# Performance work log

Hardware: AMD Instinct MI355X
Metric: run time of the kernel (lower is better)

Reference implementation:

```python
import jax, jax.numpy as jnp
import numpy as np

CL = 32      # config.cl (latent width)
NOBJ = 32    # config.num_obj
N = 1024     # batch


def _linear_params(key, fan_in, fan_out):
    w = jax.random.normal(key, (fan_in, fan_out), dtype=jnp.float32) / np.sqrt(fan_in)
    b = jnp.full((fan_out,), 0.1, dtype=jnp.float32)
    return w, b


def setup_inputs() -> dict:
    key = jax.random.key(0)
    keys = jax.random.split(key, 16)
    inp = {"s": jax.random.normal(keys[0], (N, NOBJ, CL // 2), dtype=jnp.float32)}
    specs = [
        ("state_enc", [(CL // 2, CL)]),
        ("self", [(CL, CL), (CL, CL)]),
        ("rel", [(2 * CL + 1, 2 * CL), (2 * CL, CL), (CL, CL)]),
        ("att", [(2 * CL + 1, 2 * CL), (2 * CL, CL), (CL, 1)]),
        ("aff", [(CL, CL), (CL, CL), (CL, CL)]),
        ("out", [(2 * CL, CL), (CL, CL)]),
    ]
    k = 1
    for name, shapes in specs:
        for j, (fi, fo) in enumerate(shapes):
            w, b = _linear_params(keys[k], fi, fo)
            k += 1
            if len(shapes) == 1:
                inp[name + "_w"], inp[name + "_b"] = w, b
            else:
                inp[name + "_w" + str(j)], inp[name + "_b" + str(j)] = w, b
    inp["core_idx"] = 0
    return inp


def _forward(s, state_enc_w, state_enc_b,
             self_w0, self_b0, self_w1, self_b1,
             rel_w0, rel_b0, rel_w1, rel_b1, rel_w2, rel_b2,
             att_w0, att_b0, att_w1, att_b1, att_w2, att_b2,
             aff_w0, aff_b0, aff_w1, aff_b1, aff_w2, aff_b2,
             out_w0, out_b0, out_w1, out_b1):
    # state encoding; keep raw (x, y) positions in the first 2 channels
    enc = s @ state_enc_w + state_enc_b                      # (n, o, cl)
    s2 = jnp.concatenate([s[..., :2], enc[..., 2:]], axis=-1)  # (n, o, cl)

    # self dynamics (residual MLP)
    h1 = jax.nn.relu(s2 @ self_w0 + self_b0)
    self_dyn = h1 @ self_w1 + self_b1 + h1                   # (n, o, cl)

    # pairwise squared distance over first two channels
    pos = s2[..., :2]
    diff = pos[:, :, None, :] - pos[:, None, :, :]           # (n, o, o, 2)
    dist = jnp.sum(diff * diff, axis=-1)                     # (n, o, o)

    # first layer of the edge MLPs applied to cat(obj_i, obj_j, dist) without
    # materializing the (n, o, o, 2cl+1) concat: split weight into W_i|W_j|w_d
    def pair_first(W, b):
        a = s2 @ W[:CL]                                      # (n, o, H)
        c = s2 @ W[CL:2 * CL]                                # (n, o, H)
        return a[:, :, None, :] + c[:, None, :, :] + dist[..., None] * W[2 * CL] + b

    # relation core (residual on last layer)
    rel1 = jax.nn.relu(pair_first(rel_w0, rel_b0))           # (n, o, o, 2cl)
    rel2 = jax.nn.relu(rel1 @ rel_w1 + rel_b1)               # (n, o, o, cl)
    rel_f = rel2 @ rel_w2 + rel_b2 + rel2                    # (n, o, o, cl)

    # attention net -> exp (unnormalized attention)
    att = jax.nn.relu(pair_first(att_w0, att_b0))
    att = jax.nn.relu(att @ att_w1 + att_b1)
    att = jnp.exp(att @ att_w2 + att_b2)                     # (n, o, o, 1)

    diag_mask = (1.0 - jnp.eye(NOBJ, dtype=s2.dtype))[None, :, :, None]
    rel_dyn = jnp.sum(rel_f * diag_mask * att, axis=2)       # (n, o, cl)

    dyn = self_dyn + rel_dyn

    # affector (tanh residual MLP)
    aff1 = jnp.tanh(dyn @ aff_w0 + aff_b0)
    aff2 = jnp.tanh(aff1 @ aff_w1 + aff_b1) + aff1
    aff3 = aff2 @ aff_w2 + aff_b2

    # output head
    aff_s = jnp.concatenate([aff3, s2], axis=-1)             # (n, o, 2cl)
    o1 = jnp.tanh(aff_s @ out_w0 + out_b0)
    result = o1 @ out_w1 + out_b1 + o1                       # (n, o, cl)
    return result


def reference(s, state_enc_w, state_enc_b,
              self_w0, self_b0, self_w1, self_b1,
              rel_w0, rel_b0, rel_w1, rel_b1, rel_w2, rel_b2,
              att_w0, att_b0, att_w1, att_b1, att_w2, att_b2,
              aff_w0, aff_b0, aff_w1, aff_b1, aff_w2, aff_b2,
              out_w0, out_b0, out_w1, out_b1, core_idx):
    # core_idx selects one of 3 identical cores in the original; only core 0
    # is materialized here (forward uses a single core).
    del core_idx
    return _forward(s, state_enc_w, state_enc_b,
                    self_w0, self_b0, self_w1, self_b1,
                    rel_w0, rel_b0, rel_w1, rel_b1, rel_w2, rel_b2,
                    att_w0, att_b0, att_w1, att_b1, att_w2, att_b2,
                    aff_w0, aff_b0, aff_w1, aff_b1, aff_w2, aff_b2,
                    out_w0, out_b0, out_w1, out_b1)
```

## Files before the change

kernel.cpp:

```cpp
#include <hip/hip_runtime.h>
#include <stdint.h>


enum : int {
  ENC_W  = 0,     ENC_B  = 512,
  SELF_W0 = 544,  SELF_B0 = 1568, SELF_W1 = 1600, SELF_B1 = 2624,
  REL_W0 = 2656,  REL_B0 = 6816,  REL_W1 = 6880,  REL_B1 = 8928,
  REL_W2 = 8960,  REL_B2 = 9984,
  ATT_W0 = 10016, ATT_B0 = 14176, ATT_W1 = 14240, ATT_B1 = 16288,
  ATT_W2 = 16320, ATT_B2 = 16352,
  AFF_W0 = 16356, AFF_B0 = 17380, AFF_W1 = 17412, AFF_B1 = 18436,
  AFF_W2 = 18468, AFF_B2 = 19492,
  OUT_W0 = 19524, OUT_B0 = 21572, OUT_W1 = 21604, OUT_B1 = 22628,
  W_FLAG = 22660,
  W_TOTAL = 22661
};

__device__ __forceinline__ float bf2f(uint16_t h) {
  union { uint32_t u; float f; } v; v.u = ((uint32_t)h) << 16; return v.f;
}
__device__ __forceinline__ uint16_t f2bf(float f) {
  union { float f; uint32_t u; } v; v.f = f;
  uint32_t r = (v.u + 0x7fffu + ((v.u >> 16) & 1u)) >> 16;
  return (uint16_t)r;
}

struct ConvArgs {
  const void* src[28];
  const uint32_t* probe;
  int size[28];
  int off[28];
};

__global__ void dyn_conv_kernel(ConvArgs a, float* __restrict__ W) {
  const int t = blockIdx.x;
  const bool is_fp32 = (*a.probe == 0x3DCCCCCDu);
  const int cnt = a.size[t];
  float* d = W + a.off[t];
  if (is_fp32) {
    const float* s = (const float*)a.src[t];
    for (int e = threadIdx.x; e < cnt; e += blockDim.x) d[e] = s[e];
  } else {
    const uint16_t* s = (const uint16_t*)a.src[t];
    for (int e = threadIdx.x; e < cnt; e += blockDim.x) d[e] = bf2f(s[e]);
  }
  if (t == 0 && threadIdx.x == 0) W[W_FLAG] = is_fp32 ? 1.f : 0.f;
}

struct ArenaPair {
  float pa[32][68];
  float pc[32][68];
};
struct ArenaPost {
  float rd[32][36];
  float t1[32][36];
  float t2[32][36];
};
struct ArenaEarly {
  float s[32][16];
  float h1[32][33];
};
union ArenaU {
  ArenaPair a;
  ArenaPost b;
  ArenaEarly c;
};

__global__ __launch_bounds__(256, 2) void dyn_main_kernel(
    const void* __restrict__ Sv,
    const float* __restrict__ Wf,
    void* __restrict__ OUTv)
{
  __shared__ __align__(16) ArenaU u;
  __shared__ float sh_s2[32][33];
  __shared__ float sh_dist[32][33];
  __shared__ float sh_sd[32][33];
  __shared__ float sh_wdr[64];
  __shared__ float sh_wda[64];
  __shared__ __align__(16) float sh_wtA[2048];
  __shared__ __align__(16) float sh_wtB[2048];
  __shared__ float sh_misc[100];

  const int tid = threadIdx.x;
  const int n   = blockIdx.x;
  const int i8  = tid >> 3;
  const int l8  = tid & 7;
  const int m0  = l8 << 2;
  const int jg  = l8 & 3;
  const int h16 = (l8 >> 2) << 4;
  const int h4  = (l8 >> 2) << 2;

  const bool is_fp32 = (Wf[W_FLAG] != 0.f);

  const float4* wtA4 = (const float4*)sh_wtA;
  const float4* wtB4 = (const float4*)sh_wtB;

  auto stage = [&](float* dst, int off, int n4) {
    const float4* src = (const float4*)(Wf + off);
    float4* d4 = (float4*)dst;
    for (int q = tid; q < n4; q += 256) d4[q] = src[q];
  };

  {
    const int e = tid * 2;
    if (is_fp32) {
      const float* sp = (const float*)Sv + (size_t)n * 512;
      u.c.s[e >> 4][e & 15]             = sp[e];
      u.c.s[(e + 1) >> 4][(e + 1) & 15] = sp[e + 1];
    } else {
      const uint16_t* sp = (const uint16_t*)Sv + (size_t)n * 512;
      u.c.s[e >> 4][e & 15]             = bf2f(sp[e]);
      u.c.s[(e + 1) >> 4][(e + 1) & 15] = bf2f(sp[e + 1]);
    }
    stage(sh_wtA, ENC_W, 128);
  }
  __syncthreads();

  {
    float e0 = Wf[ENC_B + m0 + 0], e1 = Wf[ENC_B + m0 + 1];
    float e2 = Wf[ENC_B + m0 + 2], e3 = Wf[ENC_B + m0 + 3];
    #pragma unroll
    for (int c = 0; c < 16; ++c) {
      const float sc = u.c.s[i8][c];
      const float4 w = wtA4[c * 8 + l8];
      e0 = fmaf(sc, w.x, e0); e1 = fmaf(sc, w.y, e1);
      e2 = fmaf(sc, w.z, e2); e3 = fmaf(sc, w.w, e3);
    }
    if (m0 == 0) { e0 = u.c.s[i8][0]; e1 = u.c.s[i8][1]; }
    sh_s2[i8][m0 + 0] = e0; sh_s2[i8][m0 + 1] = e1;
    sh_s2[i8][m0 + 2] = e2; sh_s2[i8][m0 + 3] = e3;
    stage(sh_wtB, SELF_W0, 256);
  }
  __syncthreads();

  {
    const float xi = sh_s2[i8][0], yi = sh_s2[i8][1];
    #pragma unroll
    for (int q = 0; q < 4; ++q) {
      const int j = m0 + q;
      const float dx = xi - sh_s2[j][0];
      const float dy = yi - sh_s2[j][1];
      sh_dist[i8][j] = dx * dx + dy * dy;
    }
  }
  {
    float a0 = Wf[SELF_B0 + m0 + 0], a1 = Wf[SELF_B0 + m0 + 1];
    float a2 = Wf[SELF_B0 + m0 + 2], a3 = Wf[SELF_B0 + m0 + 3];
    #pragma unroll
    for (int k = 0; k < 32; ++k) {
      const float x = sh_s2[i8][k];
      const float4 w = wtB4[k * 8 + l8];
      a0 = fmaf(x, w.x, a0); a1 = fmaf(x, w.y, a1);
      a2 = fmaf(x, w.z, a2); a3 = fmaf(x, w.w, a3);
    }
    u.c.h1[i8][m0 + 0] = fmaxf(a0, 0.f); u.c.h1[i8][m0 + 1] = fmaxf(a1, 0.f);
    u.c.h1[i8][m0 + 2] = fmaxf(a2, 0.f); u.c.h1[i8][m0 + 3] = fmaxf(a3, 0.f);
    stage(sh_wtA, SELF_W1, 256);
  }
  __syncthreads();

  {
    float a0 = Wf[SELF_B1 + m0 + 0], a1 = Wf[SELF_B1 + m0 + 1];
    float a2 = Wf[SELF_B1 + m0 + 2], a3 = Wf[SELF_B1 + m0 + 3];
    #pragma unroll
    for (int k = 0; k < 32; ++k) {
      const float x = u.c.h1[i8][k];
      const float4 w = wtA4[k * 8 + l8];
      a0 = fmaf(x, w.x, a0); a1 = fmaf(x, w.y, a1);
      a2 = fmaf(x, w.z, a2); a3 = fmaf(x, w.w, a3);
    }
    sh_sd[i8][m0 + 0] = a0 + u.c.h1[i8][m0 + 0];
    sh_sd[i8][m0 + 1] = a1 + u.c.h1[i8][m0 + 1];
    sh_sd[i8][m0 + 2] = a2 + u.c.h1[i8][m0 + 2];
    sh_sd[i8][m0 + 3] = a3 + u.c.h1[i8][m0 + 3];
  }
  __syncthreads();

  auto precompute_ac = [&](int W0base, int B0base) {
    const int arr = tid >> 7;
    const int row = (tid >> 2) & 31;
    const int k0  = (tid & 3) * 16;
    const float* bb = Wf + B0base + k0;
    const float bs = (arr == 0) ? 1.f : 0.f;
    float acc[16];
    #pragma unroll
    for (int kk = 0; kk < 16; ++kk) acc[kk] = bs * bb[kk];
    const float* wb = Wf + W0base + arr * 2048 + k0;
    for (int c = 0; c < 32; ++c) {
      const float sc = sh_s2[row][c];
      const float* w = wb + c * 64;
      #pragma unroll
      for (int kk = 0; kk < 16; kk += 4) {
        const float4 wv = *(const float4*)&w[kk];
        acc[kk + 0] = fmaf(sc, wv.x, acc[kk + 0]);
        acc[kk + 1] = fmaf(sc, wv.y, acc[kk + 1]);
        acc[kk + 2] = fmaf(sc, wv.z, acc[kk + 2]);
        acc[kk + 3] = fmaf(sc, wv.w, acc[kk + 3]);
      }
    }
    float* dst = (arr == 0) ? &u.a.pa[row][k0] : &u.a.pc[row][k0];
    #pragma unroll
    for (int kk = 0; kk < 16; kk += 4)
      *(float4*)&dst[kk] = make_float4(acc[kk], acc[kk+1], acc[kk+2], acc[kk+3]);
  };

  if (tid < 64)        sh_wdr[tid]      = Wf[REL_W0 + 64 * 64 + tid];
  else if (tid < 128)  sh_wda[tid - 64] = Wf[ATT_W0 + 64 * 64 + (tid - 64)];
  stage(sh_wtB, ATT_W1, 512);
  if (tid < 97)
    sh_misc[tid] = Wf[tid < 32 ? REL_B1 + tid
                    : tid < 64 ? ATT_B1 + (tid - 32)
                    : tid < 96 ? ATT_W2 + (tid - 64) : ATT_B2];
  precompute_ac(ATT_W0, ATT_B0);
  __syncthreads();

  stage(sh_wtA, REL_W1, 512);
  auto att_pair2 = [&](int p) -> float2 {
    asm volatile("" ::: "memory");
    const int j1 = jg + 8 * p;
    const int j2 = jg + 4 + 8 * p;
    const float d1 = sh_dist[i8][j1];
    const float d2 = sh_dist[i8][j2];
    const float4* A  = (const float4*)&u.a.pa[i8][0];
    const float4* C1 = (const float4*)&u.a.pc[j1][0];
    const float4* C2 = (const float4*)&u.a.pc[j2][0];
    const float4* D  = (const float4*)&sh_wda[0];
    float v1[16], v2[16];
    #pragma unroll
    for (int m = 0; m < 16; ++m) { v1[m] = sh_misc[32 + h16 + m]; v2[m] = v1[m]; }
    #pragma unroll 1
    for (int kq = 0; kq < 16; ++kq) {
      const float4 av = A[kq], c1 = C1[kq], c2 = C2[kq], wv = D[kq];
      const float x0 = fmaxf(fmaf(d1, wv.x, av.x + c1.x), 0.f);
      const float x1 = fmaxf(fmaf(d1, wv.y, av.y + c1.y), 0.f);
      const float x2 = fmaxf(fmaf(d1, wv.z, av.z + c1.z), 0.f);
      const float x3 = fmaxf(fmaf(d1, wv.w, av.w + c1.w), 0.f);
      const float y0 = fmaxf(fmaf(d2, wv.x, av.x + c2.x), 0.f);
      const float y1 = fmaxf(fmaf(d2, wv.y, av.y + c2.y), 0.f);
      const float y2 = fmaxf(fmaf(d2, wv.z, av.z + c2.z), 0.f);
      const float y3 = fmaxf(fmaf(d2, wv.w, av.w + c2.w), 0.f);
      const float4* wb = wtB4 + kq * 32 + h4;
      #pragma unroll
      for (int mq = 0; mq < 4; ++mq) {
        const float4 w0 = wb[mq], w1 = wb[8+mq], w2 = wb[16+mq], w3 = wb[24+mq];
        float t;
        t = fmaf(x0, w0.x, v1[mq*4+0]); t = fmaf(x1, w1.x, t);
        t = fmaf(x2, w2.x, t);          v1[mq*4+0] = fmaf(x3, w3.x, t);
        t = fmaf(y0, w0.x, v2[mq*4+0]); t = fmaf(y1, w1.x, t);
        t = fmaf(y2, w2.x, t);          v2[mq*4+0] = fmaf(y3, w3.x, t);
        t = fmaf(x0, w0.y, v1[mq*4+1]); t = fmaf(x1, w1.y, t);
        t = fmaf(x2, w2.y, t);          v1[mq*4+1] = fmaf(x3, w3.y, t);
        t = fmaf(y0, w0.y, v2[mq*4+1]); t = fmaf(y1, w1.y, t);
        t = fmaf(y2, w2.y, t);          v2[mq*4+1] = fmaf(y3, w3.y, t);
        t = fmaf(x0, w0.z, v1[mq*4+2]); t = fmaf(x1, w1.z, t);
        t = fmaf(x2, w2.z, t);          v1[mq*4+2] = fmaf(x3, w3.z, t);
        t = fmaf(y0, w0.z, v2[mq*4+2]); t = fmaf(y1, w1.z, t);
        t = fmaf(y2, w2.z, t);          v2[mq*4+2] = fmaf(y3, w3.z, t);
        t = fmaf(x0, w0.w, v1[mq*4+3]); t = fmaf(x1, w1.w, t);
        t = fmaf(x2, w2.w, t);          v1[mq*4+3] = fmaf(x3, w3.w, t);
        t = fmaf(y0, w0.w, v2[mq*4+3]); t = fmaf(y1, w1.w, t);
        t = fmaf(y2, w2.w, t);          v2[mq*4+3] = fmaf(y3, w3.w, t);
      }
    }
    float la0 = 0.f, la1 = 0.f, lb0 = 0.f, lb1 = 0.f;
    #pragma unroll
    for (int k = 0; k < 16; k += 2) {
      la0 = fmaf(fmaxf(v1[k + 0], 0.f), sh_misc[64 + h16 + k + 0], la0);
      la1 = fmaf(fmaxf(v1[k + 1], 0.f), sh_misc[64 + h16 + k + 1], la1);
      lb0 = fmaf(fmaxf(v2[k + 0], 0.f), sh_misc[64 + h16 + k + 0], lb0);
      lb1 = fmaf(fmaxf(v2[k + 1], 0.f), sh_misc[64 + h16 + k + 1], lb1);
    }
    float lg1 = la0 + la1;
    float lg2 = lb0 + lb1;
    lg1 += __shfl_xor(lg1, 4);
    lg2 += __shfl_xor(lg2, 4);
    lg1 += sh_misc[96];
    lg2 += sh_misc[96];
    float2 r;
    r.x = (j1 == i8) ? 0.f : expf(lg1);
    r.y = (j2 == i8) ? 0.f : expf(lg2);
    return r;
  };
  const float2 ep0 = att_pair2(0);
  const float2 ep1 = att_pair2(1);
  const float2 ep2 = att_pair2(2);
  const float2 ep3 = att_pair2(3);
  float E = ((ep0.x + ep0.y) + (ep1.x + ep1.y))
          + ((ep2.x + ep2.y) + (ep3.x + ep3.y));
  __syncthreads();

  precompute_ac(REL_W0, REL_B0);
  stage(sh_wtB, REL_W2, 256);
  __syncthreads();

  float g[16];
  #pragma unroll
  for (int m = 0; m < 16; ++m) g[m] = 0.f;

  auto rel_pair2 = [&](int p, float e1, float e2) {
    asm volatile("" ::: "memory");
    const int j1 = jg + 8 * p;
    const int j2 = jg + 4 + 8 * p;
    const float d1 = sh_dist[i8][j1];
    const float d2 = sh_dist[i8][j2];
    const float4* A  = (const float4*)&u.a.pa[i8][0];
    const float4* C1 = (const float4*)&u.a.pc[j1][0];
    const float4* C2 = (const float4*)&u.a.pc[j2][0];
    const float4* D  = (const float4*)&sh_wdr[0];
    float v1[16], v2[16];
    #pragma unroll
    for (int m = 0; m < 16; ++m) { v1[m] = sh_misc[h16 + m]; v2[m] = v1[m]; }
    #pragma unroll 1
    for (int kq = 0; kq < 16; ++kq) {
      const float4 av = A[kq], c1 = C1[kq], c2 = C2[kq], wv = D[kq];
      const float x0 = fmaxf(fmaf(d1, wv.x, av.x + c1.x), 0.f);
      const float x1 = fmaxf(fmaf(d1, wv.y, av.y + c1.y), 0.f);
      const float x2 = fmaxf(fmaf(d1, wv.z, av.z + c1.z), 0.f);
      const float x3 = fmaxf(fmaf(d1, wv.w, av.w + c1.w), 0.f);
      const float y0 = fmaxf(fmaf(d2, wv.x, av.x + c2.x), 0.f);
      const float y1 = fmaxf(fmaf(d2, wv.y, av.y + c2.y), 0.f);
      const float y2 = fmaxf(fmaf(d2, wv.z, av.z + c2.z), 0.f);
      const float y3 = fmaxf(fmaf(d2, wv.w, av.w + c2.w), 0.f);
      const float4* wb = wtA4 + kq * 32 + h4;
      #pragma unroll
      for (int mq = 0; mq < 4; ++mq) {
        const float4 w0 = wb[mq], w1 = wb[8+mq], w2 = wb[16+mq], w3 = wb[24+mq];
        float t;
        t = fmaf(x0, w0.x, v1[mq*4+0]); t = fmaf(x1, w1.x, t);
        t = fmaf(x2, w2.x, t);          v1[mq*4+0] = fmaf(x3, w3.x, t);
        t = fmaf(y0, w0.x, v2[mq*4+0]); t = fmaf(y1, w1.x, t);
        t = fmaf(y2, w2.x, t);          v2[mq*4+0] = fmaf(y3, w3.x, t);
        t = fmaf(x0, w0.y, v1[mq*4+1]); t = fmaf(x1, w1.y, t);
        t = fmaf(x2, w2.y, t);          v1[mq*4+1] = fmaf(x3, w3.y, t);
        t = fmaf(y0, w0.y, v2[mq*4+1]); t = fmaf(y1, w1.y, t);
        t = fmaf(y2, w2.y, t);          v2[mq*4+1] = fmaf(y3, w3.y, t);
        t = fmaf(x0, w0.z, v1[mq*4+2]); t = fmaf(x1, w1.z, t);
        t = fmaf(x2, w2.z, t);          v1[mq*4+2] = fmaf(x3, w3.z, t);
        t = fmaf(y0, w0.z, v2[mq*4+2]); t = fmaf(y1, w1.z, t);
        t = fmaf(y2, w2.z, t);          v2[mq*4+2] = fmaf(y3, w3.z, t);
        t = fmaf(x0, w0.w, v1[mq*4+3]); t = fmaf(x1, w1.w, t);
        t = fmaf(x2, w2.w, t);          v1[mq*4+3] = fmaf(x3, w3.w, t);
        t = fmaf(y0, w0.w, v2[mq*4+3]); t = fmaf(y1, w1.w, t);
        t = fmaf(y2, w2.w, t);          v2[mq*4+3] = fmaf(y3, w3.w, t);
      }
    }
    #pragma unroll
    for (int m = 0; m < 16; ++m) {
      g[m] = fmaf(e1, fmaxf(v1[m], 0.f), g[m]);
      g[m] = fmaf(e2, fmaxf(v2[m], 0.f), g[m]);
    }
  };
  rel_pair2(0, ep0.x, ep0.y);
  rel_pair2(1, ep1.x, ep1.y);
  rel_pair2(2, ep2.x, ep2.y);
  rel_pair2(3, ep3.x, ep3.y);

  #pragma unroll
  for (int m = 0; m < 16; ++m) {
    float vv = g[m];
    vv += __shfl_xor(vv, 1);
    vv += __shfl_xor(vv, 2);
    g[m] = vv;
  }
  E += __shfl_xor(E, 1);
  E += __shfl_xor(E, 2);
  __syncthreads();
  if (l8 == 0) {
    #pragma unroll
    for (int q = 0; q < 4; ++q)
      *(float4*)&u.b.t1[i8][q * 4] =
          make_float4(g[q * 4], g[q * 4 + 1], g[q * 4 + 2], g[q * 4 + 3]);
    u.b.t1[i8][32] = E;
  } else if (l8 == 4) {
    #pragma unroll
    for (int q = 0; q < 4; ++q)
      *(float4*)&u.b.t1[i8][16 + q * 4] =
          make_float4(g[q * 4], g[q * 4 + 1], g[q * 4 + 2], g[q * 4 + 3]);
  }
  __syncthreads();

  {
    stage(sh_wtA, AFF_W0, 256);
    const float Ei = u.b.t1[i8][32];
    float a0 = fmaf(Ei, Wf[REL_B2 + m0 + 0], u.b.t1[i8][m0 + 0]);
    float a1 = fmaf(Ei, Wf[REL_B2 + m0 + 1], u.b.t1[i8][m0 + 1]);
    float a2 = fmaf(Ei, Wf[REL_B2 + m0 + 2], u.b.t1[i8][m0 + 2]);
    float a3 = fmaf(Ei, Wf[REL_B2 + m0 + 3], u.b.t1[i8][m0 + 3]);
    #pragma unroll
    for (int k = 0; k < 32; ++k) {
      const float x = u.b.t1[i8][k];
      const float4 w = wtB4[k * 8 + l8];
      a0 = fmaf(x, w.x, a0); a1 = fmaf(x, w.y, a1);
      a2 = fmaf(x, w.z, a2); a3 = fmaf(x, w.w, a3);
    }
    __syncthreads();
    u.b.rd[i8][m0 + 0] = a0; u.b.rd[i8][m0 + 1] = a1;
    u.b.rd[i8][m0 + 2] = a2; u.b.rd[i8][m0 + 3] = a3;
  }
  __syncthreads();

  {
    stage(sh_wtB, AFF_W1, 256);
    float a0 = Wf[AFF_B0 + m0 + 0], a1 = Wf[AFF_B0 + m0 + 1];
    float a2 = Wf[AFF_B0 + m0 + 2], a3 = Wf[AFF_B0 + m0 + 3];
    #pragma unroll
    for (int k = 0; k < 32; ++k) {
      const float x = sh_sd[i8][k] + u.b.rd[i8][k];
      const float4 w = wtA4[k * 8 + l8];
      a0 = fmaf(x, w.x, a0); a1 = fmaf(x, w.y, a1);
      a2 = fmaf(x, w.z, a2); a3 = fmaf(x, w.w, a3);
    }
    u.b.t1[i8][m0 + 0] = tanhf(a0); u.b.t1[i8][m0 + 1] = tanhf(a1);
    u.b.t1[i8][m0 + 2] = tanhf(a2); u.b.t1[i8][m0 + 3] = tanhf(a3);
  }
  __syncthreads();

  {
    stage(sh_wtA, AFF_W2, 256);
    float a0 = Wf[AFF_B1 + m0 + 0], a1 = Wf[AFF_B1 + m0 + 1];
    float a2 = Wf[AFF_B1 + m0 + 2], a3 = Wf[AFF_B1 + m0 + 3];
    #pragma unroll
    for (int k = 0; k < 32; ++k) {
      const float x = u.b.t1[i8][k];
      const float4 w = wtB4[k * 8 + l8];
      a0 = fmaf(x, w.x, a0); a1 = fmaf(x, w.y, a1);
      a2 = fmaf(x, w.z, a2); a3 = fmaf(x, w.w, a3);
    }
    u.b.t2[i8][m0 + 0] = tanhf(a0) + u.b.t1[i8][m0 + 0];
    u.b.t2[i8][m0 + 1] = tanhf(a1) + u.b.t1[i8][m0 + 1];
    u.b.t2[i8][m0 + 2] = tanhf(a2) + u.b.t1[i8][m0 + 2];
    u.b.t2[i8][m0 + 3] = tanhf(a3) + u.b.t1[i8][m0 + 3];
  }
  __syncthreads();

  {
    stage(sh_wtB, OUT_W0, 512);
    float a0 = Wf[AFF_B2 + m0 + 0], a1 = Wf[AFF_B2 + m0 + 1];
    float a2 = Wf[AFF_B2 + m0 + 2], a3 = Wf[AFF_B2 + m0 + 3];
    #pragma unroll
    for (int k = 0; k < 32; ++k) {
      const float x = u.b.t2[i8][k];
      const float4 w = wtA4[k * 8 + l8];
      a0 = fmaf(x, w.x, a0); a1 = fmaf(x, w.y, a1);
      a2 = fmaf(x, w.z, a2); a3 = fmaf(x, w.w, a3);
    }
    u.b.t1[i8][m0 + 0] = a0; u.b.t1[i8][m0 + 1] = a1;
    u.b.t1[i8][m0 + 2] = a2; u.b.t1[i8][m0 + 3] = a3;
  }
  __syncthreads();

  {
    stage(sh_wtA, OUT_W1, 256);
    float a0 = Wf[OUT_B0 + m0 + 0], a1 = Wf[OUT_B0 + m0 + 1];
    float a2 = Wf[OUT_B0 + m0 + 2], a3 = Wf[OUT_B0 + m0 + 3];
    #pragma unroll
    for (int k = 0; k < 32; ++k) {
      const float x1 = u.b.t1[i8][k];
      const float4 wa = wtB4[k * 8 + l8];
      a0 = fmaf(x1, wa.x, a0); a1 = fmaf(x1, wa.y, a1);
      a2 = fmaf(x1, wa.z, a2); a3 = fmaf(x1, wa.w, a3);
      const float x2 = sh_s2[i8][k];
      const float4 wbv = wtB4[256 + k * 8 + l8];
      a0 = fmaf(x2, wbv.x, a0); a1 = fmaf(x2, wbv.y, a1);
      a2 = fmaf(x2, wbv.z, a2); a3 = fmaf(x2, wbv.w, a3);
    }
    u.b.t2[i8][m0 + 0] = tanhf(a0); u.b.t2[i8][m0 + 1] = tanhf(a1);
    u.b.t2[i8][m0 + 2] = tanhf(a2); u.b.t2[i8][m0 + 3] = tanhf(a3);
  }
  __syncthreads();

  {
    float a0 = Wf[OUT_B1 + m0 + 0], a1 = Wf[OUT_B1 + m0 + 1];
    float a2 = Wf[OUT_B1 + m0 + 2], a3 = Wf[OUT_B1 + m0 + 3];
    #pragma unroll
    for (int k = 0; k < 32; ++k) {
      const float x = u.b.t2[i8][k];
      const float4 w = wtA4[k * 8 + l8];
      a0 = fmaf(x, w.x, a0); a1 = fmaf(x, w.y, a1);
      a2 = fmaf(x, w.z, a2); a3 = fmaf(x, w.w, a3);
    }
    a0 += u.b.t2[i8][m0 + 0]; a1 += u.b.t2[i8][m0 + 1];
    a2 += u.b.t2[i8][m0 + 2]; a3 += u.b.t2[i8][m0 + 3];
    const size_t idx = (size_t)n * 1024 + i8 * 32 + m0;
    if (is_fp32) {
      *(float4*)&((float*)OUTv)[idx] = make_float4(a0, a1, a2, a3);
    } else {
      ushort4 r;
      r.x = f2bf(a0); r.y = f2bf(a1); r.z = f2bf(a2); r.w = f2bf(a3);
      *(ushort4*)&((uint16_t*)OUTv)[idx] = r;
    }
  }
}

extern "C" void kernel_launch(void* const* d_in, const int* in_sizes, int n_in,
                              void* d_out, int out_size, void* d_ws, size_t ws_size,
                              hipStream_t stream) {
  (void)in_sizes; (void)n_in; (void)out_size; (void)ws_size;
  static const int sizes[28] = {
    512, 32, 1024, 32, 1024, 32,
    4160, 64, 2048, 32, 1024, 32,
    4160, 64, 2048, 32, 32, 1,
    1024, 32, 1024, 32, 1024, 32,
    2048, 32, 1024, 32};
  static const int offs[28] = {
    ENC_W, ENC_B, SELF_W0, SELF_B0, SELF_W1, SELF_B1,
    REL_W0, REL_B0, REL_W1, REL_B1, REL_W2, REL_B2,
    ATT_W0, ATT_B0, ATT_W1, ATT_B1, ATT_W2, ATT_B2,
    AFF_W0, AFF_B0, AFF_W1, AFF_B1, AFF_W2, AFF_B2,
    OUT_W0, OUT_B0, OUT_W1, OUT_B1};

  ConvArgs ca;
  for (int i = 0; i < 28; ++i) {
    ca.src[i]  = d_in[1 + i];
    ca.size[i] = sizes[i];
    ca.off[i]  = offs[i];
  }
  ca.probe = (const uint32_t*)d_in[2];
  float* W = (float*)d_ws;
  hipLaunchKernelGGL(dyn_conv_kernel, dim3(28), dim3(256), 0, stream, ca, W);
  hipLaunchKernelGGL(dyn_main_kernel, dim3(1024), dim3(256), 0, stream,
                     d_in[0], (const float*)W, d_out);
}
```

Before: 324.1 us.

## Split fused kernel into pairwise and tail kernels via workspace

Splits the single fused per-batch kernel into two. The first computes the encoding, self dynamics and the attention-weighted pairwise aggregation, writing s2, self_dyn, g and E to global workspace. The second reads these back and runs the rel/aff/out MLP tail. The aim is to shrink shared memory and register footprint per kernel so occupancy improves, at the cost of an extra launch and about 12 MB of global traffic. The original fused kernel is kept as a fallback when the workspace is too small.

```diff
diff --git a/kernel.cpp b/kernel.cpp
--- a/kernel.cpp
+++ b/kernel.cpp
@@ -15,6 +15,14 @@
   W_FLAG = 22660,
   W_TOTAL = 22661
 };
+enum : int {
+  WS_S2 = 22664,
+  WS_SD = WS_S2 + 1048576,
+  WS_G  = WS_SD + 1048576,
+  WS_E  = WS_G  + 1048576,
+  WS_TOTAL_F = WS_E + 32768
+};
+static const size_t WS_NEED_BYTES = (size_t)WS_TOTAL_F * 4;
 
 __device__ __forceinline__ float bf2f(uint16_t h) {
   union { uint32_t u; float f; } v; v.u = ((uint32_t)h) << 16; return v.f;
@@ -66,15 +74,13 @@
   ArenaEarly c;
 };
 
-__global__ __launch_bounds__(256, 2) void dyn_main_kernel(
-    const void* __restrict__ Sv,
-    const float* __restrict__ Wf,
-    void* __restrict__ OUTv)
+__global__ __launch_bounds__(256, 2) void dyn_pair_kernel(
+    const void* __restrict__ Sv, const float* __restrict__ Wf,
+    float* __restrict__ WS)
 {
   __shared__ __align__(16) ArenaU u;
   __shared__ float sh_s2[32][33];
   __shared__ float sh_dist[32][33];
-  __shared__ float sh_sd[32][33];
   __shared__ float sh_wdr[64];
   __shared__ float sh_wda[64];
   __shared__ __align__(16) float sh_wtA[2048];
@@ -91,7 +97,6 @@
   const int h4  = (l8 >> 2) << 2;
 
   const bool is_fp32 = (Wf[W_FLAG] != 0.f);
-
   const float4* wtA4 = (const float4*)sh_wtA;
   const float4* wtB4 = (const float4*)sh_wtB;
 
@@ -129,6 +134,8 @@
     if (m0 == 0) { e0 = u.c.s[i8][0]; e1 = u.c.s[i8][1]; }
     sh_s2[i8][m0 + 0] = e0; sh_s2[i8][m0 + 1] = e1;
     sh_s2[i8][m0 + 2] = e2; sh_s2[i8][m0 + 3] = e3;
+    *(float4*)&WS[WS_S2 + (size_t)n * 1024 + i8 * 32 + m0] =
+        make_float4(e0, e1, e2, e3);
     stage(sh_wtB, SELF_W0, 256);
   }
   __syncthreads();
@@ -169,10 +176,9 @@
       a0 = fmaf(x, w.x, a0); a1 = fmaf(x, w.y, a1);
       a2 = fmaf(x, w.z, a2); a3 = fmaf(x, w.w, a3);
     }
-    sh_sd[i8][m0 + 0] = a0 + u.c.h1[i8][m0 + 0];
-    sh_sd[i8][m0 + 1] = a1 + u.c.h1[i8][m0 + 1];
-    sh_sd[i8][m0 + 2] = a2 + u.c.h1[i8][m0 + 2];
-    sh_sd[i8][m0 + 3] = a3 + u.c.h1[i8][m0 + 3];
+    *(float4*)&WS[WS_SD + (size_t)n * 1024 + i8 * 32 + m0] =
+        make_float4(a0 + u.c.h1[i8][m0 + 0], a1 + u.c.h1[i8][m0 + 1],
+                    a2 + u.c.h1[i8][m0 + 2], a3 + u.c.h1[i8][m0 + 3]);
   }
   __syncthreads();
 
@@ -290,7 +296,6 @@
   __syncthreads();
 
   precompute_ac(REL_W0, REL_B0);
-  stage(sh_wtB, REL_W2, 256);
   __syncthreads();
 
   float g[16];
@@ -364,6 +369,469 @@
   }
   E += __shfl_xor(E, 1);
   E += __shfl_xor(E, 2);
+  if (l8 == 0) {
+    #pragma unroll
+    for (int q = 0; q < 4; ++q)
+      *(float4*)&WS[WS_G + (size_t)n * 1024 + i8 * 32 + q * 4] =
+          make_float4(g[q * 4], g[q * 4 + 1], g[q * 4 + 2], g[q * 4 + 3]);
+    WS[WS_E + n * 32 + i8] = E;
+  } else if (l8 == 4) {
+    #pragma unroll
+    for (int q = 0; q < 4; ++q)
+      *(float4*)&WS[WS_G + (size_t)n * 1024 + i8 * 32 + 16 + q * 4] =
+          make_float4(g[q * 4], g[q * 4 + 1], g[q * 4 + 2], g[q * 4 + 3]);
+  }
+}
+
+__global__ __launch_bounds__(256, 2) void dyn_tail_kernel(
+    const float* __restrict__ Wf, const float* __restrict__ WS,
+    void* __restrict__ OUTv)
+{
+  __shared__ __align__(16) ArenaPost b;
+  __shared__ float sh_s2[32][33];
+  __shared__ float sh_sd[32][33];
+  __shared__ __align__(16) float sh_wtA[2048];
+  __shared__ __align__(16) float sh_wtB[2048];
+
+  const int tid = threadIdx.x;
+  const int n   = blockIdx.x;
+  const int i8  = tid >> 3;
+  const int l8  = tid & 7;
+  const int m0  = l8 << 2;
+
+  const bool is_fp32 = (Wf[W_FLAG] != 0.f);
+  const float4* wtA4 = (const float4*)sh_wtA;
+  const float4* wtB4 = (const float4*)sh_wtB;
+
+  auto stage = [&](float* dst, int off, int n4) {
+    const float4* src = (const float4*)(Wf + off);
+    float4* d4 = (float4*)dst;
+    for (int q = tid; q < n4; q += 256) d4[q] = src[q];
+  };
+
+  {
+    const int idx = tid << 2;
+    const int ii = idx >> 5, kk = idx & 31;
+    const float4 vs = *(const float4*)&WS[WS_S2 + (size_t)n * 1024 + idx];
+    sh_s2[ii][kk + 0] = vs.x; sh_s2[ii][kk + 1] = vs.y;
+    sh_s2[ii][kk + 2] = vs.z; sh_s2[ii][kk + 3] = vs.w;
+    const float4 vd = *(const float4*)&WS[WS_SD + (size_t)n * 1024 + idx];
+    sh_sd[ii][kk + 0] = vd.x; sh_sd[ii][kk + 1] = vd.y;
+    sh_sd[ii][kk + 2] = vd.z; sh_sd[ii][kk + 3] = vd.w;
+    const float4 vg = *(const float4*)&WS[WS_G + (size_t)n * 1024 + idx];
+    b.t1[ii][kk + 0] = vg.x; b.t1[ii][kk + 1] = vg.y;
+    b.t1[ii][kk + 2] = vg.z; b.t1[ii][kk + 3] = vg.w;
+    if (tid < 32) b.t1[tid][32] = WS[WS_E + n * 32 + tid];
+    stage(sh_wtB, REL_W2, 256);
+  }
+  __syncthreads();
+
+  {
+    stage(sh_wtA, AFF_W0, 256);
+    const float Ei = b.t1[i8][32];
+    float a0 = fmaf(Ei, Wf[REL_B2 + m0 + 0], b.t1[i8][m0 + 0]);
+    float a1 = fmaf(Ei, Wf[REL_B2 + m0 + 1], b.t1[i8][m0 + 1]);
+    float a2 = fmaf(Ei, Wf[REL_B2 + m0 + 2], b.t1[i8][m0 + 2]);
+    float a3 = fmaf(Ei, Wf[REL_B2 + m0 + 3], b.t1[i8][m0 + 3]);
+    #pragma unroll
+    for (int k = 0; k < 32; ++k) {
+      const float x = b.t1[i8][k];
+      const float4 w = wtB4[k * 8 + l8];
+      a0 = fmaf(x, w.x, a0); a1 = fmaf(x, w.y, a1);
+      a2 = fmaf(x, w.z, a2); a3 = fmaf(x, w.w, a3);
+    }
+    __syncthreads();
+    b.rd[i8][m0 + 0] = a0; b.rd[i8][m0 + 1] = a1;
+    b.rd[i8][m0 + 2] = a2; b.rd[i8][m0 + 3] = a3;
+  }
+  __syncthreads();
+
+  {
+    stage(sh_wtB, AFF_W1, 256);
+    float a0 = Wf[AFF_B0 + m0 + 0], a1 = Wf[AFF_B0 + m0 + 1];
+    float a2 = Wf[AFF_B0 + m0 + 2], a3 = Wf[AFF_B0 + m0 + 3];
+    #pragma unroll
+    for (int k = 0; k < 32; ++k) {
+      const float x = sh_sd[i8][k] + b.rd[i8][k];
+      const float4 w = wtA4[k * 8 + l8];
+      a0 = fmaf(x, w.x, a0); a1 = fmaf(x, w.y, a1);
+      a2 = fmaf(x, w.z, a2); a3 = fmaf(x, w.w, a3);
+    }
+    b.t1[i8][m0 + 0] = tanhf(a0); b.t1[i8][m0 + 1] = tanhf(a1);
+    b.t1[i8][m0 + 2] = tanhf(a2); b.t1[i8][m0 + 3] = tanhf(a3);
+  }
+  __syncthreads();
+
+  {
+    stage(sh_wtA, AFF_W2, 256);
+    float a0 = Wf[AFF_B1 + m0 + 0], a1 = Wf[AFF_B1 + m0 + 1];
+    float a2 = Wf[AFF_B1 + m0 + 2], a3 = Wf[AFF_B1 + m0 + 3];
+    #pragma unroll
+    for (int k = 0; k < 32; ++k) {
+      const float x = b.t1[i8][k];
+      const float4 w = wtB4[k * 8 + l8];
+      a0 = fmaf(x, w.x, a0); a1 = fmaf(x, w.y, a1);
+      a2 = fmaf(x, w.z, a2); a3 = fmaf(x, w.w, a3);
+    }
+    b.t2[i8][m0 + 0] = tanhf(a0) + b.t1[i8][m0 + 0];
+    b.t2[i8][m0 + 1] = tanhf(a1) + b.t1[i8][m0 + 1];
+    b.t2[i8][m0 + 2] = tanhf(a2) + b.t1[i8][m0 + 2];
+    b.t2[i8][m0 + 3] = tanhf(a3) + b.t1[i8][m0 + 3];
+  }
+  __syncthreads();
+
+  {
+    stage(sh_wtB, OUT_W0, 512);
+    float a0 = Wf[AFF_B2 + m0 + 0], a1 = Wf[AFF_B2 + m0 + 1];
+    float a2 = Wf[AFF_B2 + m0 + 2], a3 = Wf[AFF_B2 + m0 + 3];
+    #pragma unroll
+    for (int k = 0; k < 32; ++k) {
+      const float x = b.t2[i8][k];
+      const float4 w = wtA4[k * 8 + l8];
+      a0 = fmaf(x, w.x, a0); a1 = fmaf(x, w.y, a1);
+      a2 = fmaf(x, w.z, a2); a3 = fmaf(x, w.w, a3);
+    }
+    b.t1[i8][m0 + 0] = a0; b.t1[i8][m0 + 1] = a1;
+    b.t1[i8][m0 + 2] = a2; b.t1[i8][m0 + 3] = a3;
+  }
+  __syncthreads();
+
+  {
+    stage(sh_wtA, OUT_W1, 256);
+    float a0 = Wf[OUT_B0 + m0 + 0], a1 = Wf[OUT_B0 + m0 + 1];
+    float a2 = Wf[OUT_B0 + m0 + 2], a3 = Wf[OUT_B0 + m0 + 3];
+    #pragma unroll
+    for (int k = 0; k < 32; ++k) {
+      const float x1 = b.t1[i8][k];
+      const float4 wa = wtB4[k * 8 + l8];
+      a0 = fmaf(x1, wa.x, a0); a1 = fmaf(x1, wa.y, a1);
+      a2 = fmaf(x1, wa.z, a2); a3 = fmaf(x1, wa.w, a3);
+      const float x2 = sh_s2[i8][k];
+      const float4 wbv = wtB4[256 + k * 8 + l8];
+      a0 = fmaf(x2, wbv.x, a0); a1 = fmaf(x2, wbv.y, a1);
+      a2 = fmaf(x2, wbv.z, a2); a3 = fmaf(x2, wbv.w, a3);
+    }
+    b.t2[i8][m0 + 0] = tanhf(a0); b.t2[i8][m0 + 1] = tanhf(a1);
+    b.t2[i8][m0 + 2] = tanhf(a2); b.t2[i8][m0 + 3] = tanhf(a3);
+  }
+  __syncthreads();
+
+  {
+    float a0 = Wf[OUT_B1 + m0 + 0], a1 = Wf[OUT_B1 + m0 + 1];
+    float a2 = Wf[OUT_B1 + m0 + 2], a3 = Wf[OUT_B1 + m0 + 3];
+    #pragma unroll
+    for (int k = 0; k < 32; ++k) {
+      const float x = b.t2[i8][k];
+      const float4 w = wtA4[k * 8 + l8];
+      a0 = fmaf(x, w.x, a0); a1 = fmaf(x, w.y, a1);
+      a2 = fmaf(x, w.z, a2); a3 = fmaf(x, w.w, a3);
+    }
+    a0 += b.t2[i8][m0 + 0]; a1 += b.t2[i8][m0 + 1];
+    a2 += b.t2[i8][m0 + 2]; a3 += b.t2[i8][m0 + 3];
+    const size_t idx = (size_t)n * 1024 + i8 * 32 + m0;
+    if (is_fp32) {
+      *(float4*)&((float*)OUTv)[idx] = make_float4(a0, a1, a2, a3);
+    } else {
+      ushort4 r;
+      r.x = f2bf(a0); r.y = f2bf(a1); r.z = f2bf(a2); r.w = f2bf(a3);
+      *(ushort4*)&((uint16_t*)OUTv)[idx] = r;
+    }
+  }
+}
+
+__global__ __launch_bounds__(256, 2) void dyn_main_kernel(
+    const void* __restrict__ Sv, const float* __restrict__ Wf,
+    void* __restrict__ OUTv)
+{
+  __shared__ __align__(16) ArenaU u;
+  __shared__ float sh_s2[32][33];
+  __shared__ float sh_dist[32][33];
+  __shared__ float sh_sd[32][33];
+  __shared__ float sh_wdr[64];
+  __shared__ float sh_wda[64];
+  __shared__ __align__(16) float sh_wtA[2048];
+  __shared__ __align__(16) float sh_wtB[2048];
+  __shared__ float sh_misc[100];
+
+  const int tid = threadIdx.x;
+  const int n   = blockIdx.x;
+  const int i8  = tid >> 3;
+  const int l8  = tid & 7;
+  const int m0  = l8 << 2;
+  const int jg  = l8 & 3;
+  const int h16 = (l8 >> 2) << 4;
+  const int h4  = (l8 >> 2) << 2;
+
+  const bool is_fp32 = (Wf[W_FLAG] != 0.f);
+  const float4* wtA4 = (const float4*)sh_wtA;
+  const float4* wtB4 = (const float4*)sh_wtB;
+
+  auto stage = [&](float* dst, int off, int n4) {
+    const float4* src = (const float4*)(Wf + off);
+    float4* d4 = (float4*)dst;
+    for (int q = tid; q < n4; q += 256) d4[q] = src[q];
+  };
+
+  {
+    const int e = tid * 2;
+    if (is_fp32) {
+      const float* sp = (const float*)Sv + (size_t)n * 512;
+      u.c.s[e >> 4][e & 15]             = sp[e];
+      u.c.s[(e + 1) >> 4][(e + 1) & 15] = sp[e + 1];
+    } else {
+      const uint16_t* sp = (const uint16_t*)Sv + (size_t)n * 512;
+      u.c.s[e >> 4][e & 15]             = bf2f(sp[e]);
+      u.c.s[(e + 1) >> 4][(e + 1) & 15] = bf2f(sp[e + 1]);
+    }
+    stage(sh_wtA, ENC_W, 128);
+  }
+  __syncthreads();
+  {
+    float e0 = Wf[ENC_B + m0 + 0], e1 = Wf[ENC_B + m0 + 1];
+    float e2 = Wf[ENC_B + m0 + 2], e3 = Wf[ENC_B + m0 + 3];
+    #pragma unroll
+    for (int c = 0; c < 16; ++c) {
+      const float sc = u.c.s[i8][c];
+      const float4 w = wtA4[c * 8 + l8];
+      e0 = fmaf(sc, w.x, e0); e1 = fmaf(sc, w.y, e1);
+      e2 = fmaf(sc, w.z, e2); e3 = fmaf(sc, w.w, e3);
+    }
+    if (m0 == 0) { e0 = u.c.s[i8][0]; e1 = u.c.s[i8][1]; }
+    sh_s2[i8][m0 + 0] = e0; sh_s2[i8][m0 + 1] = e1;
+    sh_s2[i8][m0 + 2] = e2; sh_s2[i8][m0 + 3] = e3;
+    stage(sh_wtB, SELF_W0, 256);
+  }
+  __syncthreads();
+  {
+    const float xi = sh_s2[i8][0], yi = sh_s2[i8][1];
+    #pragma unroll
+    for (int q = 0; q < 4; ++q) {
+      const int j = m0 + q;
+      const float dx = xi - sh_s2[j][0];
+      const float dy = yi - sh_s2[j][1];
+      sh_dist[i8][j] = dx * dx + dy * dy;
+    }
+  }
+  {
+    float a0 = Wf[SELF_B0 + m0 + 0], a1 = Wf[SELF_B0 + m0 + 1];
+    float a2 = Wf[SELF_B0 + m0 + 2], a3 = Wf[SELF_B0 + m0 + 3];
+    #pragma unroll
+    for (int k = 0; k < 32; ++k) {
+      const float x = sh_s2[i8][k];
+      const float4 w = wtB4[k * 8 + l8];
+      a0 = fmaf(x, w.x, a0); a1 = fmaf(x, w.y, a1);
+      a2 = fmaf(x, w.z, a2); a3 = fmaf(x, w.w, a3);
+    }
+    u.c.h1[i8][m0 + 0] = fmaxf(a0, 0.f); u.c.h1[i8][m0 + 1] = fmaxf(a1, 0.f);
+    u.c.h1[i8][m0 + 2] = fmaxf(a2, 0.f); u.c.h1[i8][m0 + 3] = fmaxf(a3, 0.f);
+    stage(sh_wtA, SELF_W1, 256);
+  }
+  __syncthreads();
+  {
+    float a0 = Wf[SELF_B1 + m0 + 0], a1 = Wf[SELF_B1 + m0 + 1];
+    float a2 = Wf[SELF_B1 + m0 + 2], a3 = Wf[SELF_B1 + m0 + 3];
+    #pragma unroll
+    for (int k = 0; k < 32; ++k) {
+      const float x = u.c.h1[i8][k];
+      const float4 w = wtA4[k * 8 + l8];
+      a0 = fmaf(x, w.x, a0); a1 = fmaf(x, w.y, a1);
+      a2 = fmaf(x, w.z, a2); a3 = fmaf(x, w.w, a3);
+    }
+    sh_sd[i8][m0 + 0] = a0 + u.c.h1[i8][m0 + 0];
+    sh_sd[i8][m0 + 1] = a1 + u.c.h1[i8][m0 + 1];
+    sh_sd[i8][m0 + 2] = a2 + u.c.h1[i8][m0 + 2];
+    sh_sd[i8][m0 + 3] = a3 + u.c.h1[i8][m0 + 3];
+  }
+  __syncthreads();
+
+  auto precompute_ac = [&](int W0base, int B0base) {
+    const int arr = tid >> 7;
+    const int row = (tid >> 2) & 31;
+    const int k0  = (tid & 3) * 16;
+    const float* bb = Wf + B0base + k0;
+    const float bs = (arr == 0) ? 1.f : 0.f;
+    float acc[16];
+    #pragma unroll
+    for (int kk = 0; kk < 16; ++kk) acc[kk] = bs * bb[kk];
+    const float* wb = Wf + W0base + arr * 2048 + k0;
+    for (int c = 0; c < 32; ++c) {
+      const float sc = sh_s2[row][c];
+      const float* w = wb + c * 64;
+      #pragma unroll
+      for (int kk = 0; kk < 16; kk += 4) {
+        const float4 wv = *(const float4*)&w[kk];
+        acc[kk + 0] = fmaf(sc, wv.x, acc[kk + 0]);
+        acc[kk + 1] = fmaf(sc, wv.y, acc[kk + 1]);
+        acc[kk + 2] = fmaf(sc, wv.z, acc[kk + 2]);
+        acc[kk + 3] = fmaf(sc, wv.w, acc[kk + 3]);
+      }
+    }
+    float* dst = (arr == 0) ? &u.a.pa[row][k0] : &u.a.pc[row][k0];
+    #pragma unroll
+    for (int kk = 0; kk < 16; kk += 4)
+      *(float4*)&dst[kk] = make_float4(acc[kk], acc[kk+1], acc[kk+2], acc[kk+3]);
+  };
+
+  if (tid < 64)        sh_wdr[tid]      = Wf[REL_W0 + 64 * 64 + tid];
+  else if (tid < 128)  sh_wda[tid - 64] = Wf[ATT_W0 + 64 * 64 + (tid - 64)];
+  stage(sh_wtB, ATT_W1, 512);
+  if (tid < 97)
+    sh_misc[tid] = Wf[tid < 32 ? REL_B1 + tid
+                    : tid < 64 ? ATT_B1 + (tid - 32)
+                    : tid < 96 ? ATT_W2 + (tid - 64) : ATT_B2];
+  precompute_ac(ATT_W0, ATT_B0);
+  __syncthreads();
+
+  stage(sh_wtA, REL_W1, 512);
+  auto att_pair2 = [&](int p) -> float2 {
+    asm volatile("" ::: "memory");
+    const int j1 = jg + 8 * p;
+    const int j2 = jg + 4 + 8 * p;
+    const float d1 = sh_dist[i8][j1];
+    const float d2 = sh_dist[i8][j2];
+    const float4* A  = (const float4*)&u.a.pa[i8][0];
+    const float4* C1 = (const float4*)&u.a.pc[j1][0];
+    const float4* C2 = (const float4*)&u.a.pc[j2][0];
+    const float4* D  = (const float4*)&sh_wda[0];
+    float v1[16], v2[16];
+    #pragma unroll
+    for (int m = 0; m < 16; ++m) { v1[m] = sh_misc[32 + h16 + m]; v2[m] = v1[m]; }
+    #pragma unroll 1
+    for (int kq = 0; kq < 16; ++kq) {
+      const float4 av = A[kq], c1 = C1[kq], c2 = C2[kq], wv = D[kq];
+      const float x0 = fmaxf(fmaf(d1, wv.x, av.x + c1.x), 0.f);
+      const float x1 = fmaxf(fmaf(d1, wv.y, av.y + c1.y), 0.f);
+      const float x2 = fmaxf(fmaf(d1, wv.z, av.z + c1.z), 0.f);
+      const float x3 = fmaxf(fmaf(d1, wv.w, av.w + c1.w), 0.f);
+      const float y0 = fmaxf(fmaf(d2, wv.x, av.x + c2.x), 0.f);
+      const float y1 = fmaxf(fmaf(d2, wv.y, av.y + c2.y), 0.f);
+      const float y2 = fmaxf(fmaf(d2, wv.z, av.z + c2.z), 0.f);
+      const float y3 = fmaxf(fmaf(d2, wv.w, av.w + c2.w), 0.f);
+      const float4* wb = wtB4 + kq * 32 + h4;
+      #pragma unroll
+      for (int mq = 0; mq < 4; ++mq) {
+        const float4 w0 = wb[mq], w1 = wb[8+mq], w2 = wb[16+mq], w3 = wb[24+mq];
+        float t;
+        t = fmaf(x0, w0.x, v1[mq*4+0]); t = fmaf(x1, w1.x, t);
+        t = fmaf(x2, w2.x, t);          v1[mq*4+0] = fmaf(x3, w3.x, t);
+        t = fmaf(y0, w0.x, v2[mq*4+0]); t = fmaf(y1, w1.x, t);
+        t = fmaf(y2, w2.x, t);          v2[mq*4+0] = fmaf(y3, w3.x, t);
+        t = fmaf(x0, w0.y, v1[mq*4+1]); t = fmaf(x1, w1.y, t);
+        t = fmaf(x2, w2.y, t);          v1[mq*4+1] = fmaf(x3, w3.y, t);
+        t = fmaf(y0, w0.y, v2[mq*4+1]); t = fmaf(y1, w1.y, t);
+        t = fmaf(y2, w2.y, t);          v2[mq*4+1] = fmaf(y3, w3.y, t);
+        t = fmaf(x0, w0.z, v1[mq*4+2]); t = fmaf(x1, w1.z, t);
+        t = fmaf(x2, w2.z, t);          v1[mq*4+2] = fmaf(x3, w3.z, t);
+        t = fmaf(y0, w0.z, v2[mq*4+2]); t = fmaf(y1, w1.z, t);
+        t = fmaf(y2, w2.z, t);          v2[mq*4+2] = fmaf(y3, w3.z, t);
+        t = fmaf(x0, w0.w, v1[mq*4+3]); t = fmaf(x1, w1.w, t);
+        t = fmaf(x2, w2.w, t);          v1[mq*4+3] = fmaf(x3, w3.w, t);
+        t = fmaf(y0, w0.w, v2[mq*4+3]); t = fmaf(y1, w1.w, t);
+        t = fmaf(y2, w2.w, t);          v2[mq*4+3] = fmaf(y3, w3.w, t);
+      }
+    }
+    float la0 = 0.f, la1 = 0.f, lb0 = 0.f, lb1 = 0.f;
+    #pragma unroll
+    for (int k = 0; k < 16; k += 2) {
+      la0 = fmaf(fmaxf(v1[k + 0], 0.f), sh_misc[64 + h16 + k + 0], la0);
+      la1 = fmaf(fmaxf(v1[k + 1], 0.f), sh_misc[64 + h16 + k + 1], la1);
+      lb0 = fmaf(fmaxf(v2[k + 0], 0.f), sh_misc[64 + h16 + k + 0], lb0);
+      lb1 = fmaf(fmaxf(v2[k + 1], 0.f), sh_misc[64 + h16 + k + 1], lb1);
+    }
+    float lg1 = la0 + la1;
+    float lg2 = lb0 + lb1;
+    lg1 += __shfl_xor(lg1, 4);
+    lg2 += __shfl_xor(lg2, 4);
+    lg1 += sh_misc[96];
+    lg2 += sh_misc[96];
+    float2 r;
+    r.x = (j1 == i8) ? 0.f : expf(lg1);
+    r.y = (j2 == i8) ? 0.f : expf(lg2);
+    return r;
+  };
+  const float2 ep0 = att_pair2(0);
+  const float2 ep1 = att_pair2(1);
+  const float2 ep2 = att_pair2(2);
+  const float2 ep3 = att_pair2(3);
+  float E = ((ep0.x + ep0.y) + (ep1.x + ep1.y))
+          + ((ep2.x + ep2.y) + (ep3.x + ep3.y));
+  __syncthreads();
+
+  precompute_ac(REL_W0, REL_B0);
+  stage(sh_wtB, REL_W2, 256);
+  __syncthreads();
+
+  float g[16];
+  #pragma unroll
+  for (int m = 0; m < 16; ++m) g[m] = 0.f;
+
+  auto rel_pair2 = [&](int p, float e1, float e2) {
+    asm volatile("" ::: "memory");
+    const int j1 = jg + 8 * p;
+    const int j2 = jg + 4 + 8 * p;
+    const float d1 = sh_dist[i8][j1];
+    const float d2 = sh_dist[i8][j2];
+    const float4* A  = (const float4*)&u.a.pa[i8][0];
+    const float4* C1 = (const float4*)&u.a.pc[j1][0];
+    const float4* C2 = (const float4*)&u.a.pc[j2][0];
+    const float4* D  = (const float4*)&sh_wdr[0];
+    float v1[16], v2[16];
+    #pragma unroll
+    for (int m = 0; m < 16; ++m) { v1[m] = sh_misc[h16 + m]; v2[m] = v1[m]; }
+    #pragma unroll 1
+    for (int kq = 0; kq < 16; ++kq) {
+      const float4 av = A[kq], c1 = C1[kq], c2 = C2[kq], wv = D[kq];
+      const float x0 = fmaxf(fmaf(d1, wv.x, av.x + c1.x), 0.f);
+      const float x1 = fmaxf(fmaf(d1, wv.y, av.y + c1.y), 0.f);
+      const float x2 = fmaxf(fmaf(d1, wv.z, av.z + c1.z), 0.f);
+      const float x3 = fmaxf(fmaf(d1, wv.w, av.w + c1.w), 0.f);
+      const float y0 = fmaxf(fmaf(d2, wv.x, av.x + c2.x), 0.f);
+      const float y1 = fmaxf(fmaf(d2, wv.y, av.y + c2.y), 0.f);
+      const float y2 = fmaxf(fmaf(d2, wv.z, av.z + c2.z), 0.f);
+      const float y3 = fmaxf(fmaf(d2, wv.w, av.w + c2.w), 0.f);
+      const float4* wb = wtA4 + kq * 32 + h4;
+      #pragma unroll
+      for (int mq = 0; mq < 4; ++mq) {
+        const float4 w0 = wb[mq], w1 = wb[8+mq], w2 = wb[16+mq], w3 = wb[24+mq];
+        float t;
+        t = fmaf(x0, w0.x, v1[mq*4+0]); t = fmaf(x1, w1.x, t);
+        t = fmaf(x2, w2.x, t);          v1[mq*4+0] = fmaf(x3, w3.x, t);
+        t = fmaf(y0, w0.x, v2[mq*4+0]); t = fmaf(y1, w1.x, t);
+        t = fmaf(y2, w2.x, t);          v2[mq*4+0] = fmaf(y3, w3.x, t);
+        t = fmaf(x0, w0.y, v1[mq*4+1]); t = fmaf(x1, w1.y, t);
+        t = fmaf(x2, w2.y, t);          v1[mq*4+1] = fmaf(x3, w3.y, t);
+        t = fmaf(y0, w0.y, v2[mq*4+1]); t = fmaf(y1, w1.y, t);
+        t = fmaf(y2, w2.y, t);          v2[mq*4+1] = fmaf(y3, w3.y, t);
+        t = fmaf(x0, w0.z, v1[mq*4+2]); t = fmaf(x1, w1.z, t);
+        t = fmaf(x2, w2.z, t);          v1[mq*4+2] = fmaf(x3, w3.z, t);
+        t = fmaf(y0, w0.z, v2[mq*4+2]); t = fmaf(y1, w1.z, t);
+        t = fmaf(y2, w2.z, t);          v2[mq*4+2] = fmaf(y3, w3.z, t);
+        t = fmaf(x0, w0.w, v1[mq*4+3]); t = fmaf(x1, w1.w, t);
+        t = fmaf(x2, w2.w, t);          v1[mq*4+3] = fmaf(x3, w3.w, t);
+        t = fmaf(y0, w0.w, v2[mq*4+3]); t = fmaf(y1, w1.w, t);
+        t = fmaf(y2, w2.w, t);          v2[mq*4+3] = fmaf(y3, w3.w, t);
+      }
+    }
+    #pragma unroll
+    for (int m = 0; m < 16; ++m) {
+      g[m] = fmaf(e1, fmaxf(v1[m], 0.f), g[m]);
+      g[m] = fmaf(e2, fmaxf(v2[m], 0.f), g[m]);
+    }
+  };
+  rel_pair2(0, ep0.x, ep0.y);
+  rel_pair2(1, ep1.x, ep1.y);
+  rel_pair2(2, ep2.x, ep2.y);
+  rel_pair2(3, ep3.x, ep3.y);
+
+  #pragma unroll
+  for (int m = 0; m < 16; ++m) {
+    float vv = g[m];
+    vv += __shfl_xor(vv, 1);
+    vv += __shfl_xor(vv, 2);
+    g[m] = vv;
+  }
+  E += __shfl_xor(E, 1);
+  E += __shfl_xor(E, 2);
   __syncthreads();
   if (l8 == 0) {
     #pragma unroll
@@ -398,7 +866,6 @@
     u.b.rd[i8][m0 + 2] = a2; u.b.rd[i8][m0 + 3] = a3;
   }
   __syncthreads();
-
   {
     stage(sh_wtB, AFF_W1, 256);
     float a0 = Wf[AFF_B0 + m0 + 0], a1 = Wf[AFF_B0 + m0 + 1];
@@ -414,7 +881,6 @@
     u.b.t1[i8][m0 + 2] = tanhf(a2); u.b.t1[i8][m0 + 3] = tanhf(a3);
   }
   __syncthreads();
-
   {
     stage(sh_wtA, AFF_W2, 256);
     float a0 = Wf[AFF_B1 + m0 + 0], a1 = Wf[AFF_B1 + m0 + 1];
@@ -432,7 +898,6 @@
     u.b.t2[i8][m0 + 3] = tanhf(a3) + u.b.t1[i8][m0 + 3];
   }
   __syncthreads();
-
   {
     stage(sh_wtB, OUT_W0, 512);
     float a0 = Wf[AFF_B2 + m0 + 0], a1 = Wf[AFF_B2 + m0 + 1];
@@ -448,7 +913,6 @@
     u.b.t1[i8][m0 + 2] = a2; u.b.t1[i8][m0 + 3] = a3;
   }
   __syncthreads();
-
   {
     stage(sh_wtA, OUT_W1, 256);
     float a0 = Wf[OUT_B0 + m0 + 0], a1 = Wf[OUT_B0 + m0 + 1];
@@ -468,7 +932,6 @@
     u.b.t2[i8][m0 + 2] = tanhf(a2); u.b.t2[i8][m0 + 3] = tanhf(a3);
   }
   __syncthreads();
-
   {
     float a0 = Wf[OUT_B1 + m0 + 0], a1 = Wf[OUT_B1 + m0 + 1];
     float a2 = Wf[OUT_B1 + m0 + 2], a3 = Wf[OUT_B1 + m0 + 3];
@@ -495,7 +958,7 @@
 extern "C" void kernel_launch(void* const* d_in, const int* in_sizes, int n_in,
                               void* d_out, int out_size, void* d_ws, size_t ws_size,
                               hipStream_t stream) {
-  (void)in_sizes; (void)n_in; (void)out_size; (void)ws_size;
+  (void)in_sizes; (void)n_in; (void)out_size;
   static const int sizes[28] = {
     512, 32, 1024, 32, 1024, 32,
     4160, 64, 2048, 32, 1024, 32,
@@ -518,6 +981,13 @@
   ca.probe = (const uint32_t*)d_in[2];
   float* W = (float*)d_ws;
   hipLaunchKernelGGL(dyn_conv_kernel, dim3(28), dim3(256), 0, stream, ca, W);
-  hipLaunchKernelGGL(dyn_main_kernel, dim3(1024), dim3(256), 0, stream,
-                     d_in[0], (const float*)W, d_out);
+  if (ws_size >= WS_NEED_BYTES) {
+    hipLaunchKernelGGL(dyn_pair_kernel, dim3(1024), dim3(256), 0, stream,
+                       d_in[0], (const float*)W, W);
+    hipLaunchKernelGGL(dyn_tail_kernel, dim3(1024), dim3(256), 0, stream,
+                       (const float*)W, (const float*)W, d_out);
+  } else {
+    hipLaunchKernelGGL(dyn_main_kernel, dim3(1024), dim3(256), 0, stream,
+                       d_in[0], (const float*)W, d_out);
+  }
 }
```

Result: slower. 340.9 us (+5.2%).
